# Kernel optimization log

Measured on AMD Instinct MI355X. Metric: run time of the kernel, lower is better.

## Reference

```python
import jax
import jax.numpy as jnp
from jax import lax
import numpy as np

N_COLORS = 256  # n_possible_colors; classifier emits N_COLORS+1 logits (last = 'new color')
LRELU_SLOPE = 0.01  # torch nn.LeakyReLU default negative_slope


def setup_inputs() -> dict:
    key = jax.random.key(0)
    ks = jax.random.split(key, 8)
    N, E = 8192, 512
    deg = 32
    s1 = 1.0 / np.sqrt(2 * E)
    s2 = 1.0 / np.sqrt(E)
    s3 = 1.0 / np.sqrt(400)
    return {
        "embeddings": jax.random.normal(ks[0], (N, E), jnp.float32),
        "neighbors": jax.random.randint(ks[1], (N, deg), 0, N, jnp.int32),
        "W1": jax.random.normal(ks[2], (2 * E, E), jnp.float32) * s1,
        "b1": jnp.zeros((E,), jnp.float32),
        "W2": jax.random.normal(ks[3], (E, 400), jnp.float32) * s2,
        "b2": jnp.zeros((400,), jnp.float32),
        "W3": jax.random.normal(ks[4], (400, N_COLORS + 1), jnp.float32) * s3,
        "b3": jnp.zeros((N_COLORS + 1,), jnp.float32),
        "baseline": jnp.ones((), jnp.float32),
    }


def _leaky(x):
    return jnp.where(x >= 0, x, LRELU_SLOPE * x)


def reference(embeddings, neighbors, W1, b1, W2, b2, W3, b3, baseline):
    N, E = embeddings.shape
    C = N_COLORS + 1  # 257 output classes
    graph_emb = embeddings.mean(axis=0)  # torch.mean(embeddings, dim=0), constant across steps
    idx = jnp.arange(C)
    colors0 = jnp.full((N,), -1, jnp.int32).at[0].set(0)  # _assign_color(0, vertex_order[0])
    key0 = jax.random.key(42)

    def step(carry, v):
        colors, n_used, logp, key = carry
        key, sk = jax.random.split(key)
        # classifier MLP: cat(node_emb, graph_emb) -> 512 -> 400 -> 257
        x = jnp.concatenate([embeddings[v], graph_emb])  # [2E]
        h = _leaky(x @ W1 + b1)
        h = _leaky(h @ W2 + b2)
        logits = h @ W3 + b3  # [257]
        # _mask_irrelevant_colors: disable unused colors in [n_used, 256)
        irrel = (idx >= n_used) & (idx < N_COLORS)
        # _mask_colors: disable colors of already-colored neighbors (-1 = uncolored -> padded out)
        nb_c = colors[neighbors[v]]  # [deg]
        adj_mask = jnp.zeros((C + 1,), bool).at[jnp.where(nb_c < 0, C, nb_c)].set(True)[:C]
        logits = jnp.where(irrel | adj_mask, -jnp.inf, logits)
        probs = jax.nn.softmax(logits)  # classifier output
        raw = jax.random.categorical(sk, logits)  # np.random.choice(p=probs)
        chosen = jnp.where(raw == N_COLORS, n_used, raw).astype(jnp.int32)
        n_used = jnp.where(raw == N_COLORS, n_used + 1, n_used)
        colors = colors.at[v].set(chosen)
        p = probs[raw]
        logp = logp + jnp.log(p + 1e-8) - jnp.log(jnp.asarray(1e-8, p.dtype))
        return (colors, n_used, logp, key), None

    init = (colors0, jnp.int32(1), jnp.float32(0.0), key0)
    (colors, n_used, logp, _), _ = lax.scan(step, init, jnp.arange(1, N))
    loss = (n_used.astype(jnp.float32) - baseline) * logp / N
    return colors, loss
```

## Files before the change

### kernel.cpp

```cpp
#include <hip/hip_runtime.h>
#include <stdint.h>
#include <math.h>

#define NV 8192
#define EMB 512
#define CLS 257
#define DEG 32
#define TV 8
#define RSTRIDE 260

struct KP { uint32_t a, b; };

__host__ __device__ constexpr KP tfc(uint32_t k0, uint32_t k1,
                                     uint32_t x0, uint32_t x1) {
  const uint32_t ks2 = k0 ^ k1 ^ 0x1BD11BDAu;
  uint32_t v0 = x0 + k0, v1 = x1 + k1;
#define QR(r) { v0 += v1; v1 = (v1 << (r)) | (v1 >> (32 - (r))); v1 ^= v0; }
  QR(13) QR(15) QR(26) QR(6)
  v0 += k1;  v1 += ks2 + 1u;
  QR(17) QR(29) QR(16) QR(24)
  v0 += ks2; v1 += k0 + 2u;
  QR(13) QR(15) QR(26) QR(6)
  v0 += k0;  v1 += k1 + 3u;
  QR(17) QR(29) QR(16) QR(24)
  v0 += k1;  v1 += ks2 + 4u;
  QR(13) QR(15) QR(26) QR(6)
  v0 += ks2; v1 += k0 + 5u;
#undef QR
  return KP{v0, v1};
}

struct Seg { KP e[256]; };
constexpr Seg mkseg(KP s) {
  Seg g{};
  g.e[0] = s;
  for (int i = 1; i < 256; ++i) g.e[i] = tfc(g.e[i - 1].a, g.e[i - 1].b, 0u, 0u);
  return g;
}
#define NXTSEG(prev) mkseg(tfc(prev.e[255].a, prev.e[255].b, 0u, 0u))
constexpr Seg SG0 = mkseg(KP{0u, 42u});
constexpr Seg SG1 = NXTSEG(SG0);   constexpr Seg SG2 = NXTSEG(SG1);
constexpr Seg SG3 = NXTSEG(SG2);   constexpr Seg SG4 = NXTSEG(SG3);
constexpr Seg SG5 = NXTSEG(SG4);   constexpr Seg SG6 = NXTSEG(SG5);
constexpr Seg SG7 = NXTSEG(SG6);   constexpr Seg SG8 = NXTSEG(SG7);
constexpr Seg SG9 = NXTSEG(SG8);   constexpr Seg SG10 = NXTSEG(SG9);
constexpr Seg SG11 = NXTSEG(SG10); constexpr Seg SG12 = NXTSEG(SG11);
constexpr Seg SG13 = NXTSEG(SG12); constexpr Seg SG14 = NXTSEG(SG13);
constexpr Seg SG15 = NXTSEG(SG14); constexpr Seg SG16 = NXTSEG(SG15);
constexpr Seg SG17 = NXTSEG(SG16); constexpr Seg SG18 = NXTSEG(SG17);
constexpr Seg SG19 = NXTSEG(SG18); constexpr Seg SG20 = NXTSEG(SG19);
constexpr Seg SG21 = NXTSEG(SG20); constexpr Seg SG22 = NXTSEG(SG21);
constexpr Seg SG23 = NXTSEG(SG22); constexpr Seg SG24 = NXTSEG(SG23);
constexpr Seg SG25 = NXTSEG(SG24); constexpr Seg SG26 = NXTSEG(SG25);
constexpr Seg SG27 = NXTSEG(SG26); constexpr Seg SG28 = NXTSEG(SG27);
constexpr Seg SG29 = NXTSEG(SG28); constexpr Seg SG30 = NXTSEG(SG29);
constexpr Seg SG31 = NXTSEG(SG30);

struct KT { uint32_t hi[8192]; uint32_t lo[8192]; };
constexpr KT mkkt() {
  KT t{};
  const Seg* sg[32] = {
    &SG0,  &SG1,  &SG2,  &SG3,  &SG4,  &SG5,  &SG6,  &SG7,
    &SG8,  &SG9,  &SG10, &SG11, &SG12, &SG13, &SG14, &SG15,
    &SG16, &SG17, &SG18, &SG19, &SG20, &SG21, &SG22, &SG23,
    &SG24, &SG25, &SG26, &SG27, &SG28, &SG29, &SG30, &SG31 };
  for (int s = 0; s < 32; ++s)
    for (int i = 0; i < 256; ++i) {
      const int v = 1 + s * 256 + i;
      if (v < 8192) { t.hi[v] = sg[s]->e[i].a; t.lo[v] = sg[s]->e[i].b; }
    }
  return t;
}
__device__ const KT KEYS = mkkt();

__global__ __launch_bounds__(256) void colmean_part(const float* __restrict__ emb,
                                                    float* __restrict__ part) {
  const int b = blockIdx.x;
  const int t = threadIdx.x;
  for (int j = t; j < EMB; j += 256) {
    float s = 0.f;
    const int r0 = b * 128;
    for (int r = 0; r < 128; ++r) s += emb[(size_t)(r0 + r) * EMB + j];
    part[(size_t)b * EMB + j] = s;
  }
}

__global__ __launch_bounds__(256) void colmean_fin(const float* __restrict__ part,
                                                   float* __restrict__ g) {
  const int t = threadIdx.x;
  for (int j = t; j < EMB; j += 256) {
    float s = 0.f;
    for (int b = 0; b < 64; ++b) s += part[(size_t)b * EMB + j];
    g[j] = s / 8192.0f;
  }
}

__global__ __launch_bounds__(256) void mlp3i(
    const float* __restrict__ emb, const float* __restrict__ g,
    const float* __restrict__ W1, const float* __restrict__ b1,
    const float* __restrict__ W2, const float* __restrict__ b2,
    const float* __restrict__ W3, const float* __restrict__ b3,
    float* __restrict__ pl, float* __restrict__ er)
{
  __shared__ float xs[TV][68];
  __shared__ float gs[EMB];
  __shared__ float h1s[TV][EMB];
  __shared__ float h2s[TV][400];
  __shared__ float redw[TV][4];
  __shared__ float li256s[TV];
  __shared__ float mrs[TV];

  const int t  = threadIdx.x;
  const int v0 = blockIdx.x * TV;
  const int j2 = 2 * t;

  for (int j = t; j < EMB; j += 256) gs[j] = g[j];

  float accA[TV], accB[TV];
#pragma unroll
  for (int vv = 0; vv < TV; ++vv) { accA[vv] = 0.f; accB[vv] = 0.f; }

  for (int kc = 0; kc < 8; ++kc) {
    __syncthreads();
    if (t < 128) {
      const int vv = t >> 4;
      const int kk = (t & 15) << 2;
      const float4 s4 = *reinterpret_cast<const float4*>(
          &emb[(size_t)(v0 + vv) * EMB + kc * 64 + kk]);
      xs[vv][kk] = s4.x; xs[vv][kk + 1] = s4.y;
      xs[vv][kk + 2] = s4.z; xs[vv][kk + 3] = s4.w;
    }
    __syncthreads();
    float cA[TV], cB[TV];
#pragma unroll
    for (int vv = 0; vv < TV; ++vv) { cA[vv] = 0.f; cB[vv] = 0.f; }
    for (int q = 0; q < 16; ++q) {
      const int k = kc * 64 + q * 4;
      float2 w[4];
#pragma unroll
      for (int u = 0; u < 4; ++u)
        w[u] = *reinterpret_cast<const float2*>(&W1[(size_t)(k + u) * EMB + j2]);
      float4 xv[TV];
#pragma unroll
      for (int vv = 0; vv < TV; ++vv)
        xv[vv] = *reinterpret_cast<const float4*>(&xs[vv][q * 4]);
#pragma unroll
      for (int u = 0; u < 4; ++u) {
#pragma unroll
        for (int vv = 0; vv < TV; ++vv) {
          const float x = (u == 0) ? xv[vv].x : (u == 1) ? xv[vv].y
                         : (u == 2) ? xv[vv].z : xv[vv].w;
          cA[vv] = fmaf(x, w[u].x, cA[vv]);
          cB[vv] = fmaf(x, w[u].y, cB[vv]);
        }
      }
    }
#pragma unroll
    for (int vv = 0; vv < TV; ++vv) { accA[vv] += cA[vv]; accB[vv] += cB[vv]; }
  }

  float gA = 0.f, gB = 0.f;
  for (int kc = 0; kc < 8; ++kc) {
    float cgA = 0.f, cgB = 0.f;
    for (int q = 0; q < 16; ++q) {
      const int k = kc * 64 + q * 4;
      const float4 gv = *reinterpret_cast<const float4*>(&gs[k]);
      float2 w[4];
#pragma unroll
      for (int u = 0; u < 4; ++u)
        w[u] = *reinterpret_cast<const float2*>(
            &W1[(size_t)(EMB + k + u) * EMB + j2]);
      cgA = fmaf(gv.x, w[0].x, cgA); cgB = fmaf(gv.x, w[0].y, cgB);
      cgA = fmaf(gv.y, w[1].x, cgA); cgB = fmaf(gv.y, w[1].y, cgB);
      cgA = fmaf(gv.z, w[2].x, cgA); cgB = fmaf(gv.z, w[2].y, cgB);
      cgA = fmaf(gv.w, w[3].x, cgA); cgB = fmaf(gv.w, w[3].y, cgB);
    }
    gA += cgA; gB += cgB;
  }

  {
    const float bA = b1[j2], bB = b1[j2 + 1];
#pragma unroll
    for (int vv = 0; vv < TV; ++vv) {
      float hA = (accA[vv] + gA) + bA;
      float hB = (accB[vv] + gB) + bB;
      hA = (hA >= 0.f) ? hA : 0.01f * hA;
      hB = (hB >= 0.f) ? hB : 0.01f * hB;
      *reinterpret_cast<float2*>(&h1s[vv][j2]) = float2{hA, hB};
    }
  }
  __syncthreads();

  if (t < 200) {
    float a2A[TV], a2B[TV];
#pragma unroll
    for (int vv = 0; vv < TV; ++vv) { a2A[vv] = 0.f; a2B[vv] = 0.f; }
    for (int kc = 0; kc < 8; ++kc) {
      float cA[TV], cB[TV];
#pragma unroll
      for (int vv = 0; vv < TV; ++vv) { cA[vv] = 0.f; cB[vv] = 0.f; }
      for (int q = 0; q < 16; ++q) {
        const int k = kc * 64 + q * 4;
        float2 w[4];
#pragma unroll
        for (int u = 0; u < 4; ++u)
          w[u] = *reinterpret_cast<const float2*>(&W2[(size_t)(k + u) * 400 + j2]);
        float4 hv[TV];
#pragma unroll
        for (int vv = 0; vv < TV; ++vv)
          hv[vv] = *reinterpret_cast<const float4*>(&h1s[vv][k]);
#pragma unroll
        for (int u = 0; u < 4; ++u) {
#pragma unroll
          for (int vv = 0; vv < TV; ++vv) {
            const float x = (u == 0) ? hv[vv].x : (u == 1) ? hv[vv].y
                           : (u == 2) ? hv[vv].z : hv[vv].w;
            cA[vv] = fmaf(x, w[u].x, cA[vv]);
            cB[vv] = fmaf(x, w[u].y, cB[vv]);
          }
        }
      }
#pragma unroll
      for (int vv = 0; vv < TV; ++vv) { a2A[vv] += cA[vv]; a2B[vv] += cB[vv]; }
    }
    const float bA = b2[j2], bB = b2[j2 + 1];
#pragma unroll
    for (int vv = 0; vv < TV; ++vv) {
      float hA = a2A[vv] + bA;
      float hB = a2B[vv] + bB;
      hA = (hA >= 0.f) ? hA : 0.01f * hA;
      hB = (hB >= 0.f) ? hB : 0.01f * hB;
      *reinterpret_cast<float2*>(&h2s[vv][j2]) = float2{hA, hB};
    }
  }
  __syncthreads();

  float a3[TV], a3x[TV];
#pragma unroll
  for (int vv = 0; vv < TV; ++vv) { a3[vv] = 0.f; a3x[vv] = 0.f; }
  for (int kc = 0; kc < 8; ++kc) {
    float c3[TV], c3x[TV];
#pragma unroll
    for (int vv = 0; vv < TV; ++vv) { c3[vv] = 0.f; c3x[vv] = 0.f; }
    for (int kk = 0; kk < 50; ++kk) {
      const int k = kc * 50 + kk;
      const float w0 = W3[(size_t)k * CLS + t];
      const float wx = (t == 0) ? W3[(size_t)k * CLS + 256] : 0.f;
#pragma unroll
      for (int vv = 0; vv < TV; ++vv) {
        const float hv = h2s[vv][k];
        c3[vv]  = fmaf(hv, w0, c3[vv]);
        c3x[vv] = fmaf(hv, wx, c3x[vv]);
      }
    }
#pragma unroll
    for (int vv = 0; vv < TV; ++vv) { a3[vv] += c3[vv]; a3x[vv] += c3x[vv]; }
  }

  const float bj = b3[t];
  float li_[TV];
#pragma unroll
  for (int vv = 0; vv < TV; ++vv) li_[vv] = a3[vv] + bj;

#pragma unroll
  for (int vv = 0; vv < TV; ++vv) {
    float m = li_[vv];
#pragma unroll
    for (int off = 1; off < 64; off <<= 1) m = fmaxf(m, __shfl_xor(m, off));
    if ((t & 63) == 0) redw[vv][t >> 6] = m;
  }
  if (t == 0) {
    const float bx = b3[256];
#pragma unroll
    for (int vv = 0; vv < TV; ++vv) li256s[vv] = a3x[vv] + bx;
  }
  __syncthreads();
  if (t < TV) {
    const float m = fmaxf(fmaxf(redw[t][0], redw[t][1]),
                          fmaxf(redw[t][2], redw[t][3]));
    mrs[t] = fmaxf(m, li256s[t]);
  }
  __syncthreads();

#pragma unroll
  for (int vv = 0; vv < TV; ++vv) {
    const int v = v0 + vv;
    const float li = li_[vv];
    const KP sk = tfc(KEYS.hi[v], KEYS.lo[v], 0u, 1u);
    const KP o  = tfc(sk.a, sk.b, 0u, (uint32_t)t);
    const uint32_t bb = o.a ^ o.b;
    const float f = __uint_as_float(0x3f800000u | (bb >> 9)) - 1.0f;
    const float u = fmaxf(1.17549435e-38f, f);
    const float gg = -logf(-logf(u));
    pl[(size_t)v * RSTRIDE + t] = li + gg;
    er[(size_t)v * RSTRIDE + t] = expf(li - mrs[vv]);
  }
  if (t == 0) {
    const float bx = b3[256];
#pragma unroll
    for (int vv = 0; vv < TV; ++vv) {
      const int v = v0 + vv;
      const float li = a3x[vv] + bx;
      const KP sk = tfc(KEYS.hi[v], KEYS.lo[v], 0u, 1u);
      const KP o  = tfc(sk.a, sk.b, 0u, 256u);
      const uint32_t bb = o.a ^ o.b;
      const float f = __uint_as_float(0x3f800000u | (bb >> 9)) - 1.0f;
      const float u = fmaxf(1.17549435e-38f, f);
      const float gg = -logf(-logf(u));
      pl[(size_t)v * RSTRIDE + 256] = li + gg;
      er[(size_t)v * RSTRIDE + 256] = expf(li - mrs[vv]);
    }
  }
}

#define DPPF(CTRL, OLDI, X) \
  __builtin_amdgcn_update_dpp((int)(OLDI), (X), (CTRL), 0xF, 0xF, false)
#define SRED(CTRL) { S += __int_as_float(DPPF(CTRL, 0, __float_as_int(S))); }

__device__ __forceinline__ uint32_t ordmap(float f) {
  const uint32_t s = __float_as_uint(f);
  return s ^ (0x80000000u | (uint32_t)((int32_t)s >> 31));
}

#define WG_SCOPE __HIP_MEMORY_SCOPE_WORKGROUP

__global__ __launch_bounds__(256) void sortrows(float* __restrict__ plbuf) {
  __shared__ uint64_t keys[4][512];
  const int t = threadIdx.x;
  const int w = t >> 6;
  const int lane = t & 63;
  const int v = blockIdx.x * 4 + w;
  const float* row = plbuf + (size_t)v * RSTRIDE;

#pragma unroll
  for (int j = 0; j < 8; ++j) {
    const int i = lane + 64 * j;
    uint32_t om = 0u;
    if (i < CLS) om = ordmap(row[i]);
    keys[w][i] = ((uint64_t)om << 9) | (uint64_t)(511 - i);
  }
  __syncthreads();

  for (int k = 2; k <= 512; k <<= 1) {
    for (int j = k >> 1; j > 0; j >>= 1) {
#pragma unroll
      for (int m = 0; m < 4; ++m) {
        const int p  = lane + 64 * m;
        const int i  = ((p & ~(j - 1)) << 1) | (p & (j - 1));
        const int ix = i | j;
        const uint64_t a = keys[w][i], b = keys[w][ix];
        const bool sw = ((i & k) == 0) ? (a < b) : (a > b);
        if (sw) { keys[w][i] = b; keys[w][ix] = a; }
      }
      __syncthreads();
    }
  }

  uint16_t* o16 = reinterpret_cast<uint16_t*>(plbuf) + (size_t)v * (RSTRIDE * 2);
#pragma unroll
  for (int j = 0; j < 5; ++j) {
    const int i = lane + 64 * j;
    if (i < 320) o16[i] = (uint16_t)(511u - (uint32_t)(keys[w][i] & 511u));
  }
}

#define CRIT12(ROW, C0, C1, W0, W1, NUV, BX, BY, BZ, SLPTR, RAWV) {            \
    const bool ok0_ = (!((W0 >> (C0 & 31)) & 1u)) && (C0 < NUV || C0 == 256)   \
                   && C0 != BX && C0 != BY && C0 != BZ;                        \
    const bool ok1_ = (!((W1 >> (C1 & 31)) & 1u)) && (C1 < NUV || C1 == 256)   \
                   && C1 != BX && C1 != BY && C1 != BZ;                        \
    uint64_t b_ = __ballot(ok0_ || ok1_);                                      \
    if (b_) {                                                                  \
      const int sel_ = ok0_ ? C0 : C1;                                         \
      RAWV = __builtin_amdgcn_readlane(sel_, (int)__builtin_ctzll(b_));        \
    } else {                                                                   \
      const int sB_ = ((ROW) & 31) * 320;                                      \
      const int x2_ = scR16[sB_ + 128 + lane];                                 \
      const int x3_ = scR16[sB_ + 192 + lane];                                 \
      const int x4_ = scR16[sB_ + 256 + lane];                                 \
      const unsigned q2_ = SLPTR[x2_ >> 5];                                    \
      const unsigned q3_ = SLPTR[x3_ >> 5];                                    \
      const unsigned q4_ = SLPTR[x4_ >> 5];                                    \
      const bool o2_ = (!((q2_ >> (x2_ & 31)) & 1u)) && (x2_ < NUV || x2_ == 256) \
                    && x2_ != BX && x2_ != BY && x2_ != BZ;                    \
      const bool o3_ = (!((q3_ >> (x3_ & 31)) & 1u)) && (x3_ < NUV || x3_ == 256) \
                    && x3_ != BX && x3_ != BY && x3_ != BZ;                    \
      const bool o4_ = (!((q4_ >> (x4_ & 31)) & 1u)) && (x4_ < NUV || x4_ == 256) \
                    && x4_ != BX && x4_ != BY && x4_ != BZ;                    \
      if ((b_ = __ballot(o2_)))                                                \
        RAWV = __builtin_amdgcn_readlane(x2_, (int)__builtin_ctzll(b_));       \
      else if ((b_ = __ballot(o3_)))                                           \
        RAWV = __builtin_amdgcn_readlane(x3_, (int)__builtin_ctzll(b_));       \
      else if ((b_ = __ballot(o4_)))                                           \
        RAWV = __builtin_amdgcn_readlane(x4_, (int)__builtin_ctzll(b_));       \
    }                                                                          \
  }

#define PREP12(RA, PAR) {                                                      \
    const int ra_ = (RA);                                                      \
    const int rb_ = (ra_ + 1 < NV) ? ra_ + 1 : NV - 1;                         \
    while (pdc <= (rb_ >> 3))                                                  \
      pdc = __hip_atomic_load(&prod_done, __ATOMIC_ACQUIRE, WG_SCOPE);         \
    const uint32_t cwA_ = scR[ra_ & 31][lane];                                 \
    const uint32_t cwB_ = scR[rb_ & 31][lane];                                 \
    const int nbA_ = nbrRing[(((ra_ >> 3) & 3) << 8) + ((ra_ & 7) << 5) + ln32]; \
    const int nbB_ = nbrRing[(((rb_ >> 3) & 3) << 8) + ((rb_ & 7) << 5) + ln32]; \
    unsigned* const slA_ = bbufW[wid][PAR][0];                                 \
    unsigned* const slB_ = bbufW[wid][PAR][1];                                 \
    slA_[lane & 15] = 0u; slB_[lane & 15] = 0u;                                \
    const int cga_ = colors[nbA_];                                             \
    const int cgb_ = colors[nbB_];                                             \
    aF1 = (__ballot(nbA_ == ra_ - 1) != 0ULL);                                 \
    aF2 = (__ballot(nbA_ == ra_ - 2) != 0ULL);                                 \
    bFo = (__ballot(nbB_ == ra_) != 0ULL);                                     \
    bF1 = (__ballot(nbB_ == ra_ - 1) != 0ULL);                                 \
    bF2 = (__ballot(nbB_ == ra_ - 2) != 0ULL);                                 \
    if (cga_ >= 0) atomicOr(&slA_[cga_ >> 5], 1u << (cga_ & 31));              \
    if (cgb_ >= 0) atomicOr(&slB_[cgb_ >> 5], 1u << (cgb_ & 31));              \
    cA0 = (int)(cwA_ & 0xFFFFu); cA1 = (int)(cwA_ >> 16);                      \
    cB0 = (int)(cwB_ & 0xFFFFu); cB1 = (int)(cwB_ >> 16);                      \
    wA0 = slA_[cA0 >> 5]; wA1 = slA_[cA1 >> 5];                                \
    wB0 = slB_[cB0 >> 5]; wB1 = slB_[cB1 >> 5];                                \
  }

__global__ __launch_bounds__(192) void scan12(
    const int* __restrict__ nbrG, const uint32_t* __restrict__ scG,
    unsigned* __restrict__ rawnu, float* __restrict__ out)
{
  __shared__ int colors[NV];
  __shared__ uint32_t scR[32][160];
  __shared__ int nbrRing[1024];
  __shared__ unsigned bbufW[2][2][2][16];
  __shared__ int prod_done, consA_done, consB_done;
  __shared__ unsigned relayW[2];

  const int t = threadIdx.x;
  const int wid = t >> 6;
  const int lane = t & 63;
  const int ln32 = lane & 31;
  const uint16_t* scR16 = reinterpret_cast<const uint16_t*>(&scR[0][0]);

  for (int i = t; i < NV; i += 192) colors[i] = -1;
  if (t == 0) {
    colors[0] = 0; prod_done = 0; consA_done = 0; consB_done = 0;
    relayW[0] = 0u;
    relayW[1] = (0u << 10) | 1u;
  }
  __syncthreads();

  if (wid == 2) {
    for (int pc = 0; pc < 1024; ++pc) {
      for (;;) {
        const int ca = __hip_atomic_load(&consA_done, __ATOMIC_ACQUIRE, WG_SCOPE);
        const int cb = __hip_atomic_load(&consB_done, __ATOMIC_ACQUIRE, WG_SCOPE);
        if ((ca < cb ? ca : cb) >= pc - 3) break;
        __builtin_amdgcn_s_sleep(1);
      }
      uint32_t x[8], y[8], z[8];
#pragma unroll
      for (int r = 0; r < 8; ++r) {
        const size_t base = (size_t)(pc * 8 + r) * RSTRIDE;
        x[r] = scG[base + lane];
        y[r] = scG[base + 64 + lane];
        z[r] = (lane < 32) ? scG[base + 128 + lane] : 0u;
      }
      const int4 nb4 = *reinterpret_cast<const int4*>(nbrG + pc * 256 + 4 * lane);
#pragma unroll
      for (int r = 0; r < 8; ++r) {
        const int slot = (pc * 8 + r) & 31;
        scR[slot][lane] = x[r];
        scR[slot][64 + lane] = y[r];
        if (lane < 32) scR[slot][128 + lane] = z[r];
      }
      *reinterpret_cast<int4*>(&nbrRing[((pc & 3) << 8) + 4 * lane]) = nb4;
      if (lane == 0)
        __hip_atomic_store(&prod_done, pc + 1, __ATOMIC_RELEASE, WG_SCOPE);
    }
    return;
  }

  int pdc = 0;
  while (pdc < 1)
    pdc = __hip_atomic_load(&prod_done, __ATOMIC_ACQUIRE, WG_SCOPE);

  int cA0, cA1, cB0, cB1;
  unsigned wA0, wA1, wB0, wB1;
  bool aF1, aF2, bFo, bF1, bF2;

  int va = 1 + 2 * wid;
  PREP12(va, (va >> 2) & 1)
  if (wid == 0) { aF1 = false; aF2 = false; bF1 = false; bF2 = false; }

  for (; va < NV; va += 4) {
    const bool hasB = (va + 1 < NV);
    const int vb = hasB ? va + 1 : va;

    unsigned w1_;
    do {
      w1_ = __hip_atomic_load(&relayW[1], __ATOMIC_ACQUIRE, WG_SCOPE);
    } while ((int)(w1_ >> 10) != va - 1);
    const unsigned w0_ = relayW[0];
    const int nu   = (int)(w1_ & 0x3FFu);
    const int cpP1 = (int)(w0_ & 0x1FFu);
    const int cpP2 = (int)((w0_ >> 9) & 0x1FFu);

    unsigned* const slA = bbufW[wid][(va >> 2) & 1][0];
    unsigned* const slB = bbufW[wid][(va >> 2) & 1][1];

    const int BA1 = aF1 ? cpP2 : 511;
    const int BA2 = aF2 ? cpP1 : 511;
    int rawA = 256;
    CRIT12(va, cA0, cA1, wA0, wA1, nu, BA1, BA2, 511, slA, rawA)
    const bool newA = (rawA == 256);
    const int chosenA = newA ? nu : rawA;
    const int nu1 = nu + (newA ? 1 : 0);

    int rawB = 256, chosenB = chosenA, nu2 = nu1;
    if (hasB) {
      const int BB0 = bFo ? chosenA : 511;
      const int BB1 = bF1 ? cpP2 : 511;
      const int BB2 = bF2 ? cpP1 : 511;
      CRIT12(vb, cB0, cB1, wB0, wB1, nu1, BB0, BB1, BB2, slB, rawB)
      const bool newB = (rawB == 256);
      chosenB = newB ? nu1 : rawB;
      nu2 = nu1 + (newB ? 1 : 0);
    }

    if (lane == 0) {
      colors[va] = chosenA;
      rawnu[va] = (unsigned)rawA | ((unsigned)nu << 16);
      if (hasB) {
        colors[vb] = chosenB;
        rawnu[vb] = (unsigned)rawB | ((unsigned)nu1 << 16);
      }
      relayW[0] = (unsigned)chosenA | ((unsigned)chosenB << 9);
      __hip_atomic_store(&relayW[1],
          ((unsigned)vb << 10) | (unsigned)nu2, __ATOMIC_RELEASE, WG_SCOPE);
      const int dn = (vb + 1) >> 3;
      if (wid == 0)
        __hip_atomic_store(&consA_done, dn, __ATOMIC_RELEASE, WG_SCOPE);
      else
        __hip_atomic_store(&consB_done, dn, __ATOMIC_RELEASE, WG_SCOPE);
    }

    if (va + 4 < NV) PREP12(va + 4, ((va + 4) >> 2) & 1)
  }

  if (lane == 0) {
    if (wid == 0)
      __hip_atomic_store(&consA_done, 1024, __ATOMIC_RELEASE, WG_SCOPE);
    else
      __hip_atomic_store(&consB_done, 1024, __ATOMIC_RELEASE, WG_SCOPE);
  }

  if (wid == 1)
    for (int i = lane; i < NV; i += 64) out[i] = (float)colors[i];
}

__global__ __launch_bounds__(256) void logp_part(
    const float* __restrict__ outF, const int* __restrict__ nbrG,
    const float* __restrict__ er, const unsigned* __restrict__ rawnu,
    double* __restrict__ partd)
{
  __shared__ unsigned bb[4][16];
  const int t = threadIdx.x;
  const int w = t >> 6;
  const int lane = t & 63;
  const int ln32 = lane & 31;
  const int b = blockIdx.x;

  double a = 0.0;
  for (int i = 0; i < 32; ++i) {
    const int v = b * 128 + w * 32 + i;
    if (v == 0) continue;
    const unsigned val = rawnu[v];
    const int raw = (int)(val & 0xFFFFu);
    const int nu  = (int)(val >> 16);

    bb[w][lane & 15] = 0u;
    const int u = nbrG[(size_t)v * DEG + ln32];
    const int cu = (u < v) ? (int)outF[u] : -1;
    if (cu >= 0) atomicOr(&bb[w][cu >> 5], 1u << (cu & 31));
    unsigned bwp[4];
#pragma unroll
    for (int j = 0; j < 4; ++j) bwp[j] = bb[w][(lane >> 5) + 2 * j];
    const unsigned bw8 = bb[w][8];

    const size_t base = (size_t)v * RSTRIDE;
    bool mk[4];
    float e[4];
#pragma unroll
    for (int j = 0; j < 4; ++j) {
      const int c = lane + 64 * j;
      mk[j] = (((bwp[j] >> ln32) & 1u) != 0u) || (c >= nu);
      e[j] = mk[j] ? 0.f : er[base + c];
    }
    const bool mkX = ((bw8 & 1u) != 0u);
    const float eX = er[base + 256];
    const float e4 = (!mkX && lane == 0) ? eX : 0.f;

    float S = ((e[0] + e[1]) + (e[2] + e[3])) + e4;
    SRED(0x111) SRED(0x112) SRED(0x114) SRED(0x118) SRED(0x142) SRED(0x143)
    const float Sall = __int_as_float(
        __builtin_amdgcn_readlane(__float_as_int(S), 63));

    const bool isnew = (raw == 256);
    const int jsel  = isnew ? 4 : (raw >> 6);
    const int owner = isnew ? 0 : (raw & 63);
    const float cand = (jsel == 0) ? e[0] : (jsel == 1) ? e[1]
                     : (jsel == 2) ? e[2] : (jsel == 3) ? e[3] : e4;
    const float praw = __int_as_float(
        __builtin_amdgcn_readlane(__float_as_int(cand), owner));

    const float p = praw / Sall;
    a += (double)(logf(p + 1e-8f) - logf(1e-8f));
  }
  if (lane == 0) partd[b * 4 + w] = a;
}

__global__ __launch_bounds__(64) void finalize(
    const double* __restrict__ partd, const unsigned* __restrict__ rawnu,
    const float* __restrict__ baseline, float* __restrict__ out)
{
  if (threadIdx.x == 0) {
    double lp = 0.0;
    for (int i = 0; i < 256; ++i) lp += partd[i];
    const unsigned val = rawnu[NV - 1];
    const unsigned nf = (val >> 16) + (((val & 0xFFFFu) == 256u) ? 1u : 0u);
    out[NV] = ((float)nf - baseline[0]) * (float)lp / 8192.0f;
  }
}

extern "C" void kernel_launch(void* const* d_in, const int* in_sizes, int n_in,
                              void* d_out, int out_size, void* d_ws, size_t ws_size,
                              hipStream_t stream) {
  const float* emb      = (const float*)d_in[0];
  const int*   nbr      = (const int*)d_in[1];
  const float* W1       = (const float*)d_in[2];
  const float* b1       = (const float*)d_in[3];
  const float* W2       = (const float*)d_in[4];
  const float* b2       = (const float*)d_in[5];
  const float* W3       = (const float*)d_in[6];
  const float* b3       = (const float*)d_in[7];
  const float* baseline = (const float*)d_in[8];
  float* out = (float*)d_out;

  char* ws = (char*)d_ws;
  float* g     = (float*)ws;
  float* plbuf = (float*)(ws + 2048);
  float* erbuf = (float*)(ws + 2048 + NV * RSTRIDE * 4);
  float* part  = erbuf;
  unsigned* rawnu = (unsigned*)(ws + 2048);
  double*   partd = (double*)(ws + 2048 + 65536);

  colmean_part<<<64, 256, 0, stream>>>(emb, part);
  colmean_fin<<<1, 256, 0, stream>>>(part, g);
  mlp3i<<<NV / TV, 256, 0, stream>>>(emb, g, W1, b1, W2, b2, W3, b3, plbuf, erbuf);
  sortrows<<<NV / 4, 256, 0, stream>>>(plbuf);
  scan12<<<1, 192, 0, stream>>>(nbr, (const uint32_t*)plbuf, rawnu, out);
  logp_part<<<64, 256, 0, stream>>>((const float*)out, nbr, erbuf, rawnu, partd);
  finalize<<<1, 64, 0, stream>>>(partd, rawnu, baseline, out);
}
```

Before: 2.964 ms.

## Use four single-vertex consumer waves in sequential scan instead of two paired waves

The serial color-sampling scan now runs with four consumer waves, each handling one vertex in round-robin, plus one producer wave, instead of two consumer waves that each resolved a pair of vertices. Each wave prepares its next vertex's neighbor mask while the other three are on the critical path, and the relay word now carries the last three chosen colors for intra-window conflict checks. The aim is to shorten the per-vertex critical path by removing the second dependent CRIT evaluation per handoff. The cost is one cross-wave handoff per vertex rather than per pair, which adds latency, and the producer now polls four completion counters.

```diff
diff --git a/kernel.cpp b/kernel.cpp
--- a/kernel.cpp
+++ b/kernel.cpp
@@ -364,7 +364,7 @@
   }
 }
 
-#define CRIT12(ROW, C0, C1, W0, W1, NUV, BX, BY, BZ, SLPTR, RAWV) {            \
+#define CRIT13(ROW, C0, C1, W0, W1, NUV, BX, BY, BZ, SLPTR, RAWV) {            \
     const bool ok0_ = (!((W0 >> (C0 & 31)) & 1u)) && (C0 < NUV || C0 == 256)   \
                    && C0 != BX && C0 != BY && C0 != BZ;                        \
     const bool ok1_ = (!((W1 >> (C1 & 31)) & 1u)) && (C1 < NUV || C1 == 256)   \
@@ -396,42 +396,31 @@
     }                                                                          \
   }
 
-#define PREP12(RA, PAR) {                                                      \
-    const int ra_ = (RA);                                                      \
-    const int rb_ = (ra_ + 1 < NV) ? ra_ + 1 : NV - 1;                         \
-    while (pdc <= (rb_ >> 3))                                                  \
+#define PREP13(V) {                                                            \
+    const int v_ = (V);                                                        \
+    while (pdc <= (v_ >> 3))                                                   \
       pdc = __hip_atomic_load(&prod_done, __ATOMIC_ACQUIRE, WG_SCOPE);         \
-    const uint32_t cwA_ = scR[ra_ & 31][lane];                                 \
-    const uint32_t cwB_ = scR[rb_ & 31][lane];                                 \
-    const int nbA_ = nbrRing[(((ra_ >> 3) & 3) << 8) + ((ra_ & 7) << 5) + ln32]; \
-    const int nbB_ = nbrRing[(((rb_ >> 3) & 3) << 8) + ((rb_ & 7) << 5) + ln32]; \
-    unsigned* const slA_ = bbufW[wid][PAR][0];                                 \
-    unsigned* const slB_ = bbufW[wid][PAR][1];                                 \
-    slA_[lane & 15] = 0u; slB_[lane & 15] = 0u;                                \
-    const int cga_ = colors[nbA_];                                             \
-    const int cgb_ = colors[nbB_];                                             \
-    aF1 = (__ballot(nbA_ == ra_ - 1) != 0ULL);                                 \
-    aF2 = (__ballot(nbA_ == ra_ - 2) != 0ULL);                                 \
-    bFo = (__ballot(nbB_ == ra_) != 0ULL);                                     \
-    bF1 = (__ballot(nbB_ == ra_ - 1) != 0ULL);                                 \
-    bF2 = (__ballot(nbB_ == ra_ - 2) != 0ULL);                                 \
-    if (cga_ >= 0) atomicOr(&slA_[cga_ >> 5], 1u << (cga_ & 31));              \
-    if (cgb_ >= 0) atomicOr(&slB_[cgb_ >> 5], 1u << (cgb_ & 31));              \
-    cA0 = (int)(cwA_ & 0xFFFFu); cA1 = (int)(cwA_ >> 16);                      \
-    cB0 = (int)(cwB_ & 0xFFFFu); cB1 = (int)(cwB_ >> 16);                      \
-    wA0 = slA_[cA0 >> 5]; wA1 = slA_[cA1 >> 5];                                \
-    wB0 = slB_[cB0 >> 5]; wB1 = slB_[cB1 >> 5];                                \
-  }
-
-__global__ __launch_bounds__(192) void scan12(
+    const uint32_t cw_ = scR[v_ & 31][lane];                                   \
+    const int nb_ = nbrRing[(((v_ >> 3) & 3) << 8) + ((v_ & 7) << 5) + ln32];  \
+    sl[lane & 15] = 0u;                                                        \
+    const int cg_ = colors[nb_];                                               \
+    f1 = (__ballot(nb_ == v_ - 1) != 0ULL);                                    \
+    f2 = (__ballot(nb_ == v_ - 2) != 0ULL);                                    \
+    f3 = (__ballot(nb_ == v_ - 3) != 0ULL);                                    \
+    if (cg_ >= 0) atomicOr(&sl[cg_ >> 5], 1u << (cg_ & 31));                   \
+    c0 = (int)(cw_ & 0xFFFFu); c1 = (int)(cw_ >> 16);                          \
+    w0 = sl[c0 >> 5]; w1 = sl[c1 >> 5];                                        \
+  }
+
+__global__ __launch_bounds__(320) void scan13(
     const int* __restrict__ nbrG, const uint32_t* __restrict__ scG,
     unsigned* __restrict__ rawnu, float* __restrict__ out)
 {
   __shared__ int colors[NV];
   __shared__ uint32_t scR[32][160];
   __shared__ int nbrRing[1024];
-  __shared__ unsigned bbufW[2][2][2][16];
-  __shared__ int prod_done, consA_done, consB_done;
+  __shared__ unsigned bbufW[4][16];
+  __shared__ int prod_done, cons_done[4];
   __shared__ unsigned relayW[2];
 
   const int t = threadIdx.x;
@@ -440,20 +429,26 @@
   const int ln32 = lane & 31;
   const uint16_t* scR16 = reinterpret_cast<const uint16_t*>(&scR[0][0]);
 
-  for (int i = t; i < NV; i += 192) colors[i] = -1;
+  for (int i = t; i < NV; i += 320) colors[i] = -1;
   if (t == 0) {
-    colors[0] = 0; prod_done = 0; consA_done = 0; consB_done = 0;
-    relayW[0] = 0u;
+    colors[0] = 0; prod_done = 0;
+    cons_done[0] = 0; cons_done[1] = 0; cons_done[2] = 0; cons_done[3] = 0;
+    relayW[0] = 0u | (511u << 9) | (511u << 18);
     relayW[1] = (0u << 10) | 1u;
   }
   __syncthreads();
 
-  if (wid == 2) {
+  if (wid == 4) {
     for (int pc = 0; pc < 1024; ++pc) {
       for (;;) {
-        const int ca = __hip_atomic_load(&consA_done, __ATOMIC_ACQUIRE, WG_SCOPE);
-        const int cb = __hip_atomic_load(&consB_done, __ATOMIC_ACQUIRE, WG_SCOPE);
-        if ((ca < cb ? ca : cb) >= pc - 3) break;
+        int mn = __hip_atomic_load(&cons_done[0], __ATOMIC_ACQUIRE, WG_SCOPE);
+        const int c1_ = __hip_atomic_load(&cons_done[1], __ATOMIC_ACQUIRE, WG_SCOPE);
+        const int c2_ = __hip_atomic_load(&cons_done[2], __ATOMIC_ACQUIRE, WG_SCOPE);
+        const int c3_ = __hip_atomic_load(&cons_done[3], __ATOMIC_ACQUIRE, WG_SCOPE);
+        mn = mn < c1_ ? mn : c1_;
+        mn = mn < c2_ ? mn : c2_;
+        mn = mn < c3_ ? mn : c3_;
+        if (mn >= pc - 3) break;
         __builtin_amdgcn_s_sleep(1);
       }
       uint32_t x[8], y[8], z[8];
@@ -479,81 +474,55 @@
     return;
   }
 
+  unsigned* const sl = bbufW[wid];
   int pdc = 0;
   while (pdc < 1)
     pdc = __hip_atomic_load(&prod_done, __ATOMIC_ACQUIRE, WG_SCOPE);
 
-  int cA0, cA1, cB0, cB1;
-  unsigned wA0, wA1, wB0, wB1;
-  bool aF1, aF2, bFo, bF1, bF2;
-
-  int va = 1 + 2 * wid;
-  PREP12(va, (va >> 2) & 1)
-  if (wid == 0) { aF1 = false; aF2 = false; bF1 = false; bF2 = false; }
-
-  for (; va < NV; va += 4) {
-    const bool hasB = (va + 1 < NV);
-    const int vb = hasB ? va + 1 : va;
-
-    unsigned w1_;
+  int c0, c1;
+  unsigned w0, w1;
+  bool f1, f2, f3;
+
+  const int v0 = 1 + wid;
+  PREP13(v0)
+
+  for (int v = v0; v < NV; v += 4) {
+    unsigned w1r;
     do {
-      w1_ = __hip_atomic_load(&relayW[1], __ATOMIC_ACQUIRE, WG_SCOPE);
-    } while ((int)(w1_ >> 10) != va - 1);
-    const unsigned w0_ = relayW[0];
-    const int nu   = (int)(w1_ & 0x3FFu);
-    const int cpP1 = (int)(w0_ & 0x1FFu);
-    const int cpP2 = (int)((w0_ >> 9) & 0x1FFu);
-
-    unsigned* const slA = bbufW[wid][(va >> 2) & 1][0];
-    unsigned* const slB = bbufW[wid][(va >> 2) & 1][1];
-
-    const int BA1 = aF1 ? cpP2 : 511;
-    const int BA2 = aF2 ? cpP1 : 511;
-    int rawA = 256;
-    CRIT12(va, cA0, cA1, wA0, wA1, nu, BA1, BA2, 511, slA, rawA)
-    const bool newA = (rawA == 256);
-    const int chosenA = newA ? nu : rawA;
-    const int nu1 = nu + (newA ? 1 : 0);
-
-    int rawB = 256, chosenB = chosenA, nu2 = nu1;
-    if (hasB) {
-      const int BB0 = bFo ? chosenA : 511;
-      const int BB1 = bF1 ? cpP2 : 511;
-      const int BB2 = bF2 ? cpP1 : 511;
-      CRIT12(vb, cB0, cB1, wB0, wB1, nu1, BB0, BB1, BB2, slB, rawB)
-      const bool newB = (rawB == 256);
-      chosenB = newB ? nu1 : rawB;
-      nu2 = nu1 + (newB ? 1 : 0);
-    }
+      w1r = __hip_atomic_load(&relayW[1], __ATOMIC_ACQUIRE, WG_SCOPE);
+    } while ((int)(w1r >> 10) != v - 1);
+    const unsigned w0r = relayW[0];
+    const int nu  = (int)(w1r & 0x3FFu);
+    const int cp1 = (int)(w0r & 0x1FFu);
+    const int cp2 = (int)((w0r >> 9) & 0x1FFu);
+    const int cp3 = (int)((w0r >> 18) & 0x1FFu);
+
+    const int B1 = f1 ? cp1 : 511;
+    const int B2 = f2 ? cp2 : 511;
+    const int B3 = f3 ? cp3 : 511;
+    int raw = 256;
+    CRIT13(v, c0, c1, w0, w1, nu, B1, B2, B3, sl, raw)
+    const bool isnew = (raw == 256);
+    const int chosen = isnew ? nu : raw;
 
     if (lane == 0) {
-      colors[va] = chosenA;
-      rawnu[va] = (unsigned)rawA | ((unsigned)nu << 16);
-      if (hasB) {
-        colors[vb] = chosenB;
-        rawnu[vb] = (unsigned)rawB | ((unsigned)nu1 << 16);
-      }
-      relayW[0] = (unsigned)chosenA | ((unsigned)chosenB << 9);
+      colors[v] = chosen;
+      rawnu[v] = (unsigned)raw | ((unsigned)nu << 16);
+      relayW[0] = (unsigned)chosen | ((unsigned)cp1 << 9) | ((unsigned)cp2 << 18);
       __hip_atomic_store(&relayW[1],
-          ((unsigned)vb << 10) | (unsigned)nu2, __ATOMIC_RELEASE, WG_SCOPE);
-      const int dn = (vb + 1) >> 3;
-      if (wid == 0)
-        __hip_atomic_store(&consA_done, dn, __ATOMIC_RELEASE, WG_SCOPE);
-      else
-        __hip_atomic_store(&consB_done, dn, __ATOMIC_RELEASE, WG_SCOPE);
-    }
-
-    if (va + 4 < NV) PREP12(va + 4, ((va + 4) >> 2) & 1)
-  }
-
-  if (lane == 0) {
-    if (wid == 0)
-      __hip_atomic_store(&consA_done, 1024, __ATOMIC_RELEASE, WG_SCOPE);
-    else
-      __hip_atomic_store(&consB_done, 1024, __ATOMIC_RELEASE, WG_SCOPE);
-  }
-
-  if (wid == 1)
+          ((unsigned)v << 10) | (unsigned)(nu + (isnew ? 1 : 0)),
+          __ATOMIC_RELEASE, WG_SCOPE);
+      __hip_atomic_store(&cons_done[wid], (v + 1) >> 3,
+                         __ATOMIC_RELEASE, WG_SCOPE);
+    }
+
+    if (v + 4 < NV) PREP13(v + 4)
+  }
+
+  if (lane == 0)
+    __hip_atomic_store(&cons_done[wid], 1024, __ATOMIC_RELEASE, WG_SCOPE);
+
+  if (wid == 2)
     for (int i = lane; i < NV; i += 64) out[i] = (float)colors[i];
 }
 
@@ -657,7 +626,7 @@
   colmean_fin<<<1, 256, 0, stream>>>(part, g);
   mlp3i<<<NV / TV, 256, 0, stream>>>(emb, g, W1, b1, W2, b2, W3, b3, plbuf, erbuf);
   sortrows<<<NV / 4, 256, 0, stream>>>(plbuf);
-  scan12<<<1, 192, 0, stream>>>(nbr, (const uint32_t*)plbuf, rawnu, out);
+  scan13<<<1, 320, 0, stream>>>(nbr, (const uint32_t*)plbuf, rawnu, out);
   logp_part<<<64, 256, 0, stream>>>((const float*)out, nbr, erbuf, rawnu, partd);
   finalize<<<1, 64, 0, stream>>>(partd, rawnu, baseline, out);
 }
```

Result: slower. 3.546 ms (+19.7%).
